# Performance work log

Hardware: AMD Instinct MI355X
Metric: run time of the kernel (lower is better)

The kernel has to match this reference:

```python
import jax, jax.numpy as jnp
import numpy as np

R, D = 8192, 128                  # rays, MPI depth planes (steps per ray)
NX, NY, NZ = 160, 160, 128        # world_size (NZ == mpi_depth)
PDIM, K0, WID, PE = 16, 12, 128, 4
RGBFEA = 4 * (9 + 3 + 3 + 3) + 6  # 78, rgbnet output dim
VSR = 256.0 / D                   # voxel_size_ratio (alpha interval)
LAM = 0.01                        # glob_lambda_den / glob_lambda_rgb


def _act_shift():
    # exact replication of the act_shift buffer init in __init__
    g = np.full([D], 1.0 / D - 1e-6)
    p = [1.0 - g[0]]
    for i in range(1, D):
        p.append((1.0 - g[:i + 1].sum()) / (1.0 - g[:i].sum()))
    p = np.asarray(p)
    return jnp.asarray(np.log(p ** (-1.0 / VSR) - 1.0) - 1.0, dtype=jnp.float32)


def setup_inputs() -> dict:
    key = jax.random.key(0)
    ks = jax.random.split(key, 8)
    dim0 = 3 + 3 * PE * 2 + K0  # 39
    return {
        "rays_o": jax.random.uniform(ks[0], (R, 3), jnp.float32),
        "rays_d": jax.random.normal(ks[1], (R, 3), jnp.float32),
        "density_grid": jax.random.normal(ks[2], (1, NX, NY, NZ), jnp.float32) * 0.1,
        "density_params_grid": jax.random.normal(ks[3], (PDIM, NX, NY, NZ), jnp.float32) * 0.05,
        "k0_grid": jax.random.normal(ks[4], (K0, NX, NY, NZ), jnp.float32) * 0.1,
        "global_flow_den": jnp.zeros((2,), jnp.float32),
        "global_flow_rgb": jnp.zeros((6,), jnp.float32),
        "w0": jax.random.normal(ks[5], (dim0, WID), jnp.float32) / np.sqrt(dim0),
        "b0": jnp.zeros((WID,), jnp.float32),
        "w1": jax.random.normal(ks[6], (WID, WID), jnp.float32) / np.sqrt(WID),
        "b1": jnp.zeros((WID,), jnp.float32),
        "w2": jax.random.normal(ks[7], (WID, RGBFEA), jnp.float32) / np.sqrt(WID),
        "b2": jnp.zeros((RGBFEA,), jnp.float32),
        "act_shift": _act_shift(),  # non-trainable buffer, shape [D]
    }


def _trilinear(grid, pts):
    # grid: [C, X, Y, Z]; pts: [N, 3] in [0, 1] -> returns [N, C]
    sizes_i = np.array(grid.shape[1:], dtype=np.int32)
    sizes_f = jnp.asarray(sizes_i, dtype=pts.dtype)
    g = jnp.clip(pts, 0.0, 1.0) * (sizes_f - 1.0)
    i0 = jnp.clip(jnp.floor(g).astype(jnp.int32), 0, jnp.asarray(sizes_i - 2))
    f = g - i0.astype(pts.dtype)
    out = jnp.zeros((grid.shape[0], pts.shape[0]), dtype=pts.dtype)
    for dx in (0, 1):
        wx = f[:, 0] if dx else 1.0 - f[:, 0]
        for dy in (0, 1):
            wy = f[:, 1] if dy else 1.0 - f[:, 1]
            for dz in (0, 1):
                wz = f[:, 2] if dz else 1.0 - f[:, 2]
                v = grid[:, i0[:, 0] + dx, i0[:, 1] + dy, i0[:, 2] + dz]  # [C, N] gather
                out = out + v * (wx * wy * wz)[None, :]
    return out.T


def reference(rays_o, rays_d, density_grid, density_params_grid, k0_grid,
              global_flow_den, global_flow_rgb, w0, b0, w1, b1, w2, b2, act_shift):
    # --- packed ray sampling over MPI depth planes (create_full_step_id pattern) ---
    t = jnp.linspace(0.0, 1.0, D, dtype=rays_o.dtype)
    pts = rays_o[:, None, :] + rays_d[:, None, :] * t[None, :, None]   # [R, D, 3]
    pts = jnp.clip(pts, 0.0, 1.0).reshape(-1, 3)                        # [R*D, 3]
    ray_id = jnp.repeat(jnp.arange(R, dtype=jnp.int32), D)              # [R*D]
    step_id = jnp.tile(jnp.arange(D, dtype=jnp.int32), R)               # [R*D]

    # --- grid trilinear sampling ---
    density = _trilinear(density_grid, pts)[:, 0]          # [N]
    params = _trilinear(density_params_grid, pts)          # [N, 16]
    k0f = _trilinear(k0_grid, pts)                          # [N, 12]

    # --- per-point normalizing-flow reparam on density (4 flow steps, 4 params each) ---
    z = density + global_flow_den[0] * LAM
    for i in range(4):
        p = params[:, 4 * i:4 * i + 4]
        z = z + p[:, 0] * jnp.tanh(p[:, 1] * z + p[:, 2]) * jax.nn.sigmoid(p[:, 3])

    # --- alpha from shifted density: 1 - exp(-softplus(den + shift) * interval) ---
    den = z + act_shift[step_id]
    alpha = 1.0 - jnp.exp(-jax.nn.softplus(den) * VSR)      # [N]

    # --- per-ray transmittance via exclusive cumprod ---
    a = alpha.reshape(R, D)
    T = jnp.cumprod(1.0 - a + 1e-10, axis=1)
    T_excl = jnp.concatenate([jnp.ones((R, 1), a.dtype), T[:, :-1]], axis=1)
    weights = a * T_excl                                     # [R, D]
    alphainv_last = T[:, -1]                                 # [R]

    # --- view-direction positional encoding, broadcast per point via ray_id gather ---
    viewdirs = rays_d / (jnp.linalg.norm(rays_d, axis=-1, keepdims=True) + 1e-8)
    freq = jnp.asarray([2.0 ** i for i in range(PE)], dtype=rays_d.dtype)
    ang = viewdirs[:, :, None] * freq[None, None, :]          # [R, 3, PE]
    emb = jnp.concatenate([viewdirs, jnp.sin(ang).reshape(R, -1), jnp.cos(ang).reshape(R, -1)], -1)  # [R, 27]

    # --- MLP shading ---
    h = jnp.concatenate([emb[ray_id], k0f], axis=-1)          # [N, 39]
    h = jax.nn.relu(h @ w0 + b0)
    h = jax.nn.relu(h @ w1 + b1)
    feat = h @ w2 + b2                                        # [N, 78]
    rgb = jax.nn.sigmoid(feat[:, :3] + global_flow_rgb[:3] * LAM)  # [N, 3]

    # --- segment-sum compositing over packed ray_id (white background) ---
    wflat = weights.reshape(-1)
    rgb_marched = jax.ops.segment_sum(wflat[:, None] * rgb, ray_id, num_segments=R)
    rgb_marched = rgb_marched + alphainv_last[:, None]
    return rgb_marched
```

## Files before the change

kernel.cpp:

```cpp
#include <hip/hip_runtime.h>
#include <math.h>

#define R_    8192
#define D_    128
#define RD    (R_ * D_)
#define NXg   160
#define NYg   160
#define NZg   128
#define CSg   (NXg * NYg * NZg)
#define WIDm  128
#define K0C   12
#define LAMc  0.01f
#define VSRc  2.0f

#define W1F_N   16384
#define W0KF_N  2048
#define W2F_N   4096
#define WTAB_N  (W1F_N + W0KF_N + W2F_N)
#define LW1     0
#define LW0K    W1F_N
#define LW2     (W1F_N + W0KF_N)

typedef __attribute__((ext_vector_type(8)))  short   short8v;
typedef __attribute__((ext_vector_type(4)))  float   f32x4;
typedef __attribute__((ext_vector_type(16))) float   f32x16;
typedef __attribute__((ext_vector_type(2)))  int     int2v;
typedef __attribute__((ext_vector_type(4)))  int     int4v;
typedef __attribute__((ext_vector_type(4)))  unsigned short ushort4v;
typedef __attribute__((ext_vector_type(8)))  unsigned short ushort8v;

static __device__ __forceinline__ unsigned short f2b(float f) {
    union { float f; unsigned int u; } v; v.f = f;
    unsigned int r = v.u + 0x7fffu + ((v.u >> 16) & 1u);
    return (unsigned short)(r >> 16);
}
static __device__ __forceinline__ float b2f(unsigned short u) {
    union { unsigned int u; float f; } v; v.u = ((unsigned int)u) << 16;
    return v.f;
}
static __device__ __forceinline__ unsigned int pk2(float lo, float hi) {
    unsigned int r;
    asm("v_cvt_pk_bf16_f32 %0, %1, %2" : "=v"(r) : "v"(lo), "v"(hi));
    return r;
}
static __device__ __forceinline__ short8v as_s8(int4v v) {
    union { int4v i; short8v s; } u; u.i = v; return u.s;
}

__global__ __launch_bounds__(256) void k_pack_t(
    const float* __restrict__ dg, const float* __restrict__ pg,
    const float* __restrict__ kg, unsigned short* __restrict__ vox)
{
    const int tid = threadIdx.x;
    const int g   = tid & 3;
    const int s2  = tid >> 2;
    const float* pl[8];
    bool padq[8];
#pragma unroll
    for (int q = 0; q < 8; ++q) {
        int ch = 8 * g + q;
        padq[q] = (ch >= 29);
        pl[q] = (ch == 0) ? dg
              : (ch < 17) ? pg + (size_t)(ch - 1) * CSg
              : (ch < 29) ? kg + (size_t)(ch - 17) * CSg
              : dg;
    }
#pragma unroll
    for (int it = 0; it < 4; ++it) {
        int vofs = (blockIdx.x * 4 + it) * 256 + 4 * s2;
        f32x4 L[8];
#pragma unroll
        for (int q = 0; q < 8; ++q) {
            f32x4 v = __builtin_nontemporal_load((const f32x4*)(pl[q] + vofs));
            if (padq[q]) v = f32x4{0.0f, 0.0f, 0.0f, 0.0f};
            L[q] = v;
        }
#pragma unroll
        for (int k = 0; k < 4; ++k) {
            int4v chunk;
#pragma unroll
            for (int h2 = 0; h2 < 4; ++h2)
                chunk[h2] = (int)pk2(L[2 * h2][k], L[2 * h2 + 1][k]);
            *(int4v*)((char*)vox + (size_t)(vofs + k) * 64 + g * 16) = chunk;
        }
    }
}

__global__ __launch_bounds__(512) void k_prep_all(
    const float* __restrict__ rays_d,
    const float* __restrict__ w0, const float* __restrict__ b0,
    const float* __restrict__ w1, const float* __restrict__ w2,
    float* __restrict__ e, unsigned short* __restrict__ wtab)
{
    int bid = blockIdx.x;
    if (bid < R_ / 4) {
        int r = bid * 4 + (threadIdx.x >> 7);
        int j = threadIdx.x & 127;
        float d0 = rays_d[r * 3 + 0], d1 = rays_d[r * 3 + 1], d2 = rays_d[r * 3 + 2];
        float nrm = sqrtf(d0 * d0 + d1 * d1 + d2 * d2) + 1e-8f;
        float v[3] = { d0 / nrm, d1 / nrm, d2 / nrm };
        float x[27];
        x[0] = v[0]; x[1] = v[1]; x[2] = v[2];
#pragma unroll
        for (int c = 0; c < 3; ++c)
#pragma unroll
            for (int f = 0; f < 4; ++f) {
                float ang = v[c] * (float)(1 << f);
                x[3 + c * 4 + f]  = sinf(ang);
                x[15 + c * 4 + f] = cosf(ang);
            }
        float acc = b0[j];
#pragma unroll
        for (int m = 0; m < 27; ++m) acc = fmaf(x[m], w0[m * WIDm + j], acc);
        e[r * WIDm + j] = acc;
    } else {
        int t = (bid - R_ / 4) * 512 + threadIdx.x;
        if (t < W1F_N) {
            int tile = t >> 9, l = (t >> 3) & 63, j = t & 7;
            int mt = tile >> 3, ks = tile & 7;
            int m = mt * 32 + (l & 31);
            int k = ks * 16 + 8 * (l >> 5) + j;
            wtab[LW1 + t] = f2b(w1[k * WIDm + m]);
        } else if (t < W1F_N + W0KF_N) {
            int u = t - W1F_N;
            int mt = u >> 9, l = (u >> 3) & 63, j = u & 7;
            int m = mt * 32 + (l & 31);
            int k = 8 * (l >> 5) + j;
            wtab[LW0K + u] = f2b(k < K0C ? w0[(27 + k) * WIDm + m] : 0.0f);
        } else if (t < WTAB_N) {
            int u = t - W1F_N - W0KF_N;
            int ks = u >> 9, l = (u >> 3) & 63, j = u & 7;
            int m = l & 31;
            int k = ks * 16 + 8 * (l >> 5) + j;
            wtab[LW2 + u] = f2b(m < 3 ? w2[k * 78 + m] : 0.0f);
        }
    }
}

static __device__ __forceinline__ void sample_coords(
    int sid, const float* __restrict__ rays_o, const float* __restrict__ rays_d,
    int& ix, int& iy, int& iz, float& fx, float& fy, float& fz)
{
    int r = sid >> 7;
    int s = sid & 127;
    float t = s * (1.0f / 127.0f);
    float px = fminf(fmaxf(rays_o[r * 3 + 0] + rays_d[r * 3 + 0] * t, 0.0f), 1.0f);
    float py = fminf(fmaxf(rays_o[r * 3 + 1] + rays_d[r * 3 + 1] * t, 0.0f), 1.0f);
    float pz = fminf(fmaxf(rays_o[r * 3 + 2] + rays_d[r * 3 + 2] * t, 0.0f), 1.0f);
    float gx = px * (float)(NXg - 1);
    float gy = py * (float)(NYg - 1);
    float gz = pz * (float)(NZg - 1);
    ix = min((int)gx, NXg - 2);
    iy = min((int)gy, NYg - 2);
    iz = min((int)gz, NZg - 2);
    fx = gx - (float)ix;
    fy = gy - (float)iy;
    fz = gz - (float)iz;
}

static __device__ __forceinline__ float density_alpha(
    int s, const float* acc, float gfd0, const float* __restrict__ act_shift)
{
    float z = acc[0] + gfd0;
#pragma unroll
    for (int i = 0; i < 4; ++i) {
        float pa = acc[1 + 4 * i + 0], pb = acc[1 + 4 * i + 1];
        float pc = acc[1 + 4 * i + 2], pd = acc[1 + 4 * i + 3];
        float sg = 1.0f / (1.0f + expf(-pd));
        z += pa * tanhf(pb * z + pc) * sg;
    }
    float den = z + act_shift[s];
    float sp = fmaxf(den, 0.0f) + log1pf(expf(-fabsf(den)));
    return 1.0f - expf(-sp * VSRc);
}

static __device__ __forceinline__ void finish_sample(
    int sid, int s, const float* acc, float gfd0,
    const float* __restrict__ act_shift,
    float* __restrict__ alpha_ws, unsigned short* __restrict__ k0b)
{
    alpha_ws[sid] = density_alpha(s, acc, gfd0, act_shift);
    ushort8v lo, hi;
#pragma unroll
    for (int c = 0; c < 8; ++c) lo[c] = f2b(acc[17 + c]);
#pragma unroll
    for (int c = 0; c < 8; ++c) hi[c] = (c < 4) ? f2b(acc[25 + c]) : (unsigned short)0;
    *(ushort8v*)(k0b + (size_t)sid * 16)     = lo;
    *(ushort8v*)(k0b + (size_t)sid * 16 + 8) = hi;
}

__global__ __launch_bounds__(256) void k_gather_aos(
    const float* __restrict__ rays_o, const float* __restrict__ rays_d,
    const unsigned short* __restrict__ vox,
    const float* __restrict__ gfd, const float* __restrict__ act_shift,
    float* __restrict__ alpha_ws, unsigned short* __restrict__ k0b)
{
    int sid = blockIdx.x * 256 + threadIdx.x;
    if (sid >= RD) return;
    int ix, iy, iz; float fx, fy, fz;
    sample_coords(sid, rays_o, rays_d, ix, iy, iz, fx, fy, fz);

    const unsigned short* base = vox + ((size_t)(ix * NYg + iy) * NZg + iz) * 32;
    const size_t qoff[4] = { 0, (size_t)NZg * 32, (size_t)NYg * NZg * 32,
                             (size_t)(NYg + 1) * NZg * 32 };
    float wxy[4];
    wxy[0] = (1.0f - fx) * (1.0f - fy);
    wxy[1] = (1.0f - fx) * fy;
    wxy[2] = fx * (1.0f - fy);
    wxy[3] = fx * fy;
    float wz0 = 1.0f - fz, wz1 = fz;

    float acc[29];
#pragma unroll
    for (int c = 0; c < 29; ++c) acc[c] = 0.0f;

#pragma unroll
    for (int q = 0; q < 4; ++q) {
        const unsigned short* p = base + qoff[q];
#pragma unroll
        for (int dz = 0; dz < 2; ++dz) {
            float w = wxy[q] * (dz ? wz1 : wz0);
            const ushort8v* pv = (const ushort8v*)(p + dz * 32);
            ushort8v v0 = pv[0], v1 = pv[1], v2 = pv[2], v3 = pv[3];
#pragma unroll
            for (int i = 0; i < 8; ++i) acc[i]      = fmaf(w, b2f(v0[i]), acc[i]);
#pragma unroll
            for (int i = 0; i < 8; ++i) acc[8 + i]  = fmaf(w, b2f(v1[i]), acc[8 + i]);
#pragma unroll
            for (int i = 0; i < 8; ++i) acc[16 + i] = fmaf(w, b2f(v2[i]), acc[16 + i]);
#pragma unroll
            for (int i = 0; i < 5; ++i) acc[24 + i] = fmaf(w, b2f(v3[i]), acc[24 + i]);
        }
    }
    finish_sample(sid, sid & 127, acc, gfd[0] * LAMc, act_shift, alpha_ws, k0b);
}

__global__ void k_gather_soa(
    const float* __restrict__ rays_o, const float* __restrict__ rays_d,
    const float* __restrict__ dg,  const float* __restrict__ pg,
    const float* __restrict__ kg,  const float* __restrict__ gfd,
    const float* __restrict__ act_shift,
    float* __restrict__ alpha_ws, unsigned short* __restrict__ k0b)
{
    int sid = blockIdx.x * 256 + threadIdx.x;
    if (sid >= RD) return;
    int ix, iy, iz; float fx, fy, fz;
    sample_coords(sid, rays_o, rays_d, ix, iy, iz, fx, fy, fz);

    int base = (ix * NYg + iy) * NZg + iz;
    int off[4] = { base, base + NZg, base + NYg * NZg, base + NYg * NZg + NZg };
    float wxy[4];
    wxy[0] = (1.0f - fx) * (1.0f - fy);
    wxy[1] = (1.0f - fx) * fy;
    wxy[2] = fx * (1.0f - fy);
    wxy[3] = fx * fy;
    float wz0 = 1.0f - fz, wz1 = fz;

    auto tri = [&](const float* __restrict__ g, int c) -> float {
        float a = 0.0f;
        const float* gc = g + (size_t)c * CSg;
#pragma unroll
        for (int q = 0; q < 4; ++q) {
            const float* p = gc + off[q];
            a += (p[0] * wz0 + p[1] * wz1) * wxy[q];
        }
        return a;
    };
    float acc[29];
    acc[0] = tri(dg, 0);
#pragma unroll
    for (int c = 0; c < 16; ++c) acc[1 + c] = tri(pg, c);
#pragma unroll
    for (int c = 0; c < K0C; ++c) acc[17 + c] = tri(kg, c);
    finish_sample(sid, sid & 127, acc, gfd[0] * LAMc, act_shift, alpha_ws, k0b);
}

struct BPair { int4v lo, hi; };
static __device__ __forceinline__ BPair ttile(const f32x16 v) {
    unsigned p[8];
#pragma unroll
    for (int q = 0; q < 8; ++q) p[q] = pk2(v[2 * q], v[2 * q + 1]);
    int2v a = __builtin_amdgcn_permlane32_swap((int)p[0], (int)p[2], false, false);
    int2v b = __builtin_amdgcn_permlane32_swap((int)p[1], (int)p[3], false, false);
    int2v c = __builtin_amdgcn_permlane32_swap((int)p[4], (int)p[6], false, false);
    int2v d = __builtin_amdgcn_permlane32_swap((int)p[5], (int)p[7], false, false);
    BPair r;
    r.lo = int4v{ a.x, b.x, a.y, b.y };
    r.hi = int4v{ c.x, d.x, c.y, d.y };
    return r;
}

__global__ __launch_bounds__(256) void k_mlp_scan(
    const unsigned short* __restrict__ k0b, const float* __restrict__ e,
    const unsigned short* __restrict__ wtab,
    const float* __restrict__ b1, const float* __restrict__ b2,
    const float* __restrict__ gfr, const float* __restrict__ alpha_ws,
    float* __restrict__ out)
{
    __shared__ unsigned short wlds[WTAB_N];
    __shared__ float rgb_lds[D_][5];
#pragma unroll
    for (int it = 0; it < WTAB_N / (256 * 8); ++it) {
        int i = (it * 256 + threadIdx.x) * 8;
        *(ushort8v*)&wlds[i] = *(const ushort8v*)&wtab[i];
    }
    __syncthreads();

    const int lane = threadIdx.x & 63;
    const int wid  = threadIdx.x >> 6;
    const int n    = lane & 31;
    const int h    = lane >> 5;
    const int ray  = blockIdx.x;
    const int sid  = ray * D_ + wid * 32 + n;

    f32x16 acc0[4];
#pragma unroll
    for (int mt = 0; mt < 4; ++mt) {
        const f32x4* ep = (const f32x4*)(e + (size_t)ray * WIDm + mt * 32 + 4 * h);
#pragma unroll
        for (int rr = 0; rr < 4; ++rr) {
            f32x4 ev = ep[2 * rr];
#pragma unroll
            for (int q = 0; q < 4; ++q) acc0[mt][rr * 4 + q] = ev[q];
        }
    }
    short8v bk = *(const short8v*)(k0b + (size_t)sid * 16 + h * 8);
#pragma unroll
    for (int mt = 0; mt < 4; ++mt) {
        short8v af = *(const short8v*)&wlds[LW0K + (mt * 64 + lane) * 8];
        acc0[mt] = __builtin_amdgcn_mfma_f32_32x32x16_bf16(af, bk, acc0[mt], 0, 0, 0);
    }
    int4v bw[8];
#pragma unroll
    for (int mt = 0; mt < 4; ++mt) {
        f32x16 hv;
#pragma unroll
        for (int r = 0; r < 16; ++r) hv[r] = fmaxf(acc0[mt][r], 0.0f);
        BPair t = ttile(hv);
        bw[2 * mt]     = t.lo;
        bw[2 * mt + 1] = t.hi;
    }

    f32x16 acc1[4];
#pragma unroll
    for (int mt = 0; mt < 4; ++mt) {
        const f32x4* bp = (const f32x4*)(b1 + mt * 32 + 4 * h);
#pragma unroll
        for (int rr = 0; rr < 4; ++rr) {
            f32x4 bv = bp[2 * rr];
#pragma unroll
            for (int q = 0; q < 4; ++q) acc1[mt][rr * 4 + q] = bv[q];
        }
    }
#pragma unroll
    for (int mt = 0; mt < 4; ++mt)
#pragma unroll
        for (int ks = 0; ks < 8; ++ks) {
            short8v af = *(const short8v*)&wlds[LW1 + ((mt * 8 + ks) * 64 + lane) * 8];
            acc1[mt] = __builtin_amdgcn_mfma_f32_32x32x16_bf16(af, as_s8(bw[ks]), acc1[mt], 0, 0, 0);
        }
    int4v cw[8];
#pragma unroll
    for (int mt = 0; mt < 4; ++mt) {
        f32x16 hv;
#pragma unroll
        for (int r = 0; r < 16; ++r) hv[r] = fmaxf(acc1[mt][r], 0.0f);
        BPair t = ttile(hv);
        cw[2 * mt]     = t.lo;
        cw[2 * mt + 1] = t.hi;
    }

    f32x16 acc2;
#pragma unroll
    for (int r = 0; r < 16; ++r) acc2[r] = 0.0f;
#pragma unroll
    for (int ks = 0; ks < 8; ++ks) {
        short8v af = *(const short8v*)&wlds[LW2 + (ks * 64 + lane) * 8];
        acc2 = __builtin_amdgcn_mfma_f32_32x32x16_bf16(af, as_s8(cw[ks]), acc2, 0, 0, 0);
    }
    if (h == 0) {
#pragma unroll
        for (int c = 0; c < 3; ++c) {
            float v = acc2[c] + b2[c] + gfr[c] * LAMc;
            rgb_lds[wid * 32 + n][c] = 1.0f / (1.0f + expf(-v));
        }
    }
    __syncthreads();

    if (wid == 0) {
        int base = ray * D_ + lane * 2;
        float a0 = alpha_ws[base];
        float a1 = alpha_ws[base + 1];
        float q0 = 1.0f - a0 + 1e-10f;
        float q1 = 1.0f - a1 + 1e-10f;
        float p = q0 * q1;

        float incl = p;
#pragma unroll
        for (int o = 1; o < 64; o <<= 1) {
            float v = __shfl_up(incl, o);
            if (lane >= o) incl *= v;
        }
        float excl = __shfl_up(incl, 1);
        if (lane == 0) excl = 1.0f;
        float Tlast = __shfl(incl, 63);

        float w0s = a0 * excl;
        float w1s = a1 * excl * q0;

        float sums[3];
#pragma unroll
        for (int c = 0; c < 3; ++c) {
            float sc = w0s * rgb_lds[2 * lane][c] + w1s * rgb_lds[2 * lane + 1][c];
#pragma unroll
            for (int o = 32; o >= 1; o >>= 1) sc += __shfl_xor(sc, o);
            sums[c] = sc;
        }
        if (lane == 0) {
#pragma unroll
            for (int c = 0; c < 3; ++c) out[ray * 3 + c] = sums[c] + Tlast;
        }
    }
}

extern "C" void kernel_launch(void* const* d_in, const int* in_sizes, int n_in,
                              void* d_out, int out_size, void* d_ws, size_t ws_size,
                              hipStream_t stream) {
    const float* rays_o    = (const float*)d_in[0];
    const float* rays_d    = (const float*)d_in[1];
    const float* dg        = (const float*)d_in[2];
    const float* pg        = (const float*)d_in[3];
    const float* kg        = (const float*)d_in[4];
    const float* gfd       = (const float*)d_in[5];
    const float* gfr       = (const float*)d_in[6];
    const float* w0        = (const float*)d_in[7];
    const float* b0        = (const float*)d_in[8];
    const float* w1        = (const float*)d_in[9];
    const float* b1        = (const float*)d_in[10];
    const float* w2        = (const float*)d_in[11];
    const float* b2        = (const float*)d_in[12];
    const float* act_shift = (const float*)d_in[13];
    float* out = (float*)d_out;

    float* ws = (float*)d_ws;
    float*          alpha_ws = ws;
    unsigned short* k0b      = (unsigned short*)(ws + 4 * (size_t)RD);
    float*          e_ws     = ws + 12 * (size_t)RD;
    unsigned short* wtab     = (unsigned short*)(ws + 13 * (size_t)RD);
    size_t frag_end = 13 * (size_t)RD * 4 + (size_t)WTAB_N * 2;
    size_t vox_off  = (frag_end + 63) & ~(size_t)63;
    unsigned short* vox = (unsigned short*)((char*)d_ws + vox_off);
    size_t need = vox_off + (size_t)CSg * 64;
    bool use_aos = (ws_size >= need);

    k_prep_all<<<dim3(R_ / 4 + (WTAB_N + 511) / 512), dim3(512), 0, stream>>>(
        rays_d, w0, b0, w1, w2, e_ws, wtab);
    if (use_aos) {
        k_pack_t<<<dim3(CSg / 1024), dim3(256), 0, stream>>>(dg, pg, kg, vox);
        k_gather_aos<<<dim3(RD / 256), dim3(256), 0, stream>>>(
            rays_o, rays_d, vox, gfd, act_shift, alpha_ws, k0b);
    } else {
        k_gather_soa<<<dim3(RD / 256), dim3(256), 0, stream>>>(
            rays_o, rays_d, dg, pg, kg, gfd, act_shift, alpha_ws, k0b);
    }
    k_mlp_scan<<<dim3(R_), dim3(256), 0, stream>>>(
        k0b, e_ws, wtab, b1, b2, gfr, alpha_ws, out);
}
```

Before: 255.5 us.

## Merge pack and prep kernels; process one ray per wave in MLP

The voxel pack kernel and the embedding/weight-table prep kernel become a single launch whose block ranges select each role, removing one launch and letting the two run concurrently. The MLP/scan kernel now gives each wave one full ray and loops over four 32-sample tiles. The block-wide syncthreads and the single-wave compositing step go away, and the shared-memory weight table is loaded once per four rays instead of once per ray. In exchange, each block runs longer and serial work per wave grows, with fewer blocks available to hide latency.

```diff
diff --git a/kernel.cpp b/kernel.cpp
--- a/kernel.cpp
+++ b/kernel.cpp
@@ -21,6 +21,10 @@
 #define LW0K    W1F_N
 #define LW2     (W1F_N + W0KF_N)
 
+#define PACK_BLKS   (CSg / 1024)
+#define EPREP_BLKS  (R_ / 2)
+#define WTAB_BLKS   (WTAB_N / 256)
+
 typedef __attribute__((ext_vector_type(8)))  short   short8v;
 typedef __attribute__((ext_vector_type(4)))  float   f32x4;
 typedef __attribute__((ext_vector_type(16))) float   f32x16;
@@ -47,42 +51,103 @@
     union { int4v i; short8v s; } u; u.i = v; return u.s;
 }
 
-__global__ __launch_bounds__(256) void k_pack_t(
+static __device__ __forceinline__ void eprep_body(
+    int r, int j, const float* __restrict__ rays_d,
+    const float* __restrict__ w0, const float* __restrict__ b0, float* __restrict__ e)
+{
+    float d0 = rays_d[r * 3 + 0], d1 = rays_d[r * 3 + 1], d2 = rays_d[r * 3 + 2];
+    float nrm = sqrtf(d0 * d0 + d1 * d1 + d2 * d2) + 1e-8f;
+    float v[3] = { d0 / nrm, d1 / nrm, d2 / nrm };
+    float x[27];
+    x[0] = v[0]; x[1] = v[1]; x[2] = v[2];
+#pragma unroll
+    for (int c = 0; c < 3; ++c)
+#pragma unroll
+        for (int f = 0; f < 4; ++f) {
+            float ang = v[c] * (float)(1 << f);
+            x[3 + c * 4 + f]  = sinf(ang);
+            x[15 + c * 4 + f] = cosf(ang);
+        }
+    float acc = b0[j];
+#pragma unroll
+    for (int m = 0; m < 27; ++m) acc = fmaf(x[m], w0[m * WIDm + j], acc);
+    e[r * WIDm + j] = acc;
+}
+
+static __device__ __forceinline__ void wtab_body(
+    int t, const float* __restrict__ w0, const float* __restrict__ w1,
+    const float* __restrict__ w2, unsigned short* __restrict__ wtab)
+{
+    if (t < W1F_N) {
+        int tile = t >> 9, l = (t >> 3) & 63, j = t & 7;
+        int mt = tile >> 3, ks = tile & 7;
+        int m = mt * 32 + (l & 31);
+        int k = ks * 16 + 8 * (l >> 5) + j;
+        wtab[LW1 + t] = f2b(w1[k * WIDm + m]);
+    } else if (t < W1F_N + W0KF_N) {
+        int u = t - W1F_N;
+        int mt = u >> 9, l = (u >> 3) & 63, j = u & 7;
+        int m = mt * 32 + (l & 31);
+        int k = 8 * (l >> 5) + j;
+        wtab[LW0K + u] = f2b(k < K0C ? w0[(27 + k) * WIDm + m] : 0.0f);
+    } else if (t < WTAB_N) {
+        int u = t - W1F_N - W0KF_N;
+        int ks = u >> 9, l = (u >> 3) & 63, j = u & 7;
+        int m = l & 31;
+        int k = ks * 16 + 8 * (l >> 5) + j;
+        wtab[LW2 + u] = f2b(m < 3 ? w2[k * 78 + m] : 0.0f);
+    }
+}
+
+__global__ __launch_bounds__(256) void k_pack_prep(
     const float* __restrict__ dg, const float* __restrict__ pg,
-    const float* __restrict__ kg, unsigned short* __restrict__ vox)
-{
+    const float* __restrict__ kg, unsigned short* __restrict__ vox,
+    const float* __restrict__ rays_d,
+    const float* __restrict__ w0, const float* __restrict__ b0,
+    const float* __restrict__ w1, const float* __restrict__ w2,
+    float* __restrict__ e, unsigned short* __restrict__ wtab)
+{
+    const int bid = blockIdx.x;
     const int tid = threadIdx.x;
-    const int g   = tid & 3;
-    const int s2  = tid >> 2;
-    const float* pl[8];
-    bool padq[8];
-#pragma unroll
-    for (int q = 0; q < 8; ++q) {
-        int ch = 8 * g + q;
-        padq[q] = (ch >= 29);
-        pl[q] = (ch == 0) ? dg
-              : (ch < 17) ? pg + (size_t)(ch - 1) * CSg
-              : (ch < 29) ? kg + (size_t)(ch - 17) * CSg
-              : dg;
-    }
-#pragma unroll
-    for (int it = 0; it < 4; ++it) {
-        int vofs = (blockIdx.x * 4 + it) * 256 + 4 * s2;
-        f32x4 L[8];
+    if (bid < PACK_BLKS) {
+        const int g   = tid & 3;
+        const int s2  = tid >> 2;
+        const float* pl[8];
+        bool padq[8];
 #pragma unroll
         for (int q = 0; q < 8; ++q) {
-            f32x4 v = __builtin_nontemporal_load((const f32x4*)(pl[q] + vofs));
-            if (padq[q]) v = f32x4{0.0f, 0.0f, 0.0f, 0.0f};
-            L[q] = v;
-        }
-#pragma unroll
-        for (int k = 0; k < 4; ++k) {
-            int4v chunk;
-#pragma unroll
-            for (int h2 = 0; h2 < 4; ++h2)
-                chunk[h2] = (int)pk2(L[2 * h2][k], L[2 * h2 + 1][k]);
-            *(int4v*)((char*)vox + (size_t)(vofs + k) * 64 + g * 16) = chunk;
-        }
+            int ch = 8 * g + q;
+            padq[q] = (ch >= 29);
+            pl[q] = (ch == 0) ? dg
+                  : (ch < 17) ? pg + (size_t)(ch - 1) * CSg
+                  : (ch < 29) ? kg + (size_t)(ch - 17) * CSg
+                  : dg;
+        }
+#pragma unroll
+        for (int it = 0; it < 4; ++it) {
+            int vofs = (bid * 4 + it) * 256 + 4 * s2;
+            f32x4 L[8];
+#pragma unroll
+            for (int q = 0; q < 8; ++q) {
+                f32x4 v = __builtin_nontemporal_load((const f32x4*)(pl[q] + vofs));
+                if (padq[q]) v = f32x4{0.0f, 0.0f, 0.0f, 0.0f};
+                L[q] = v;
+            }
+#pragma unroll
+            for (int k = 0; k < 4; ++k) {
+                int4v chunk;
+#pragma unroll
+                for (int h2 = 0; h2 < 4; ++h2)
+                    chunk[h2] = (int)pk2(L[2 * h2][k], L[2 * h2 + 1][k]);
+                *(int4v*)((char*)vox + (size_t)(vofs + k) * 64 + g * 16) = chunk;
+            }
+        }
+    } else if (bid < PACK_BLKS + EPREP_BLKS) {
+        int r = (bid - PACK_BLKS) * 2 + (tid >> 7);
+        eprep_body(r, tid & 127, rays_d, w0, b0, e);
+    } else {
+        int t = (bid - PACK_BLKS - EPREP_BLKS) * 256 + tid;
+        wtab_body(t, w0, w1, w2, wtab);
     }
 }
 
@@ -95,45 +160,10 @@
     int bid = blockIdx.x;
     if (bid < R_ / 4) {
         int r = bid * 4 + (threadIdx.x >> 7);
-        int j = threadIdx.x & 127;
-        float d0 = rays_d[r * 3 + 0], d1 = rays_d[r * 3 + 1], d2 = rays_d[r * 3 + 2];
-        float nrm = sqrtf(d0 * d0 + d1 * d1 + d2 * d2) + 1e-8f;
-        float v[3] = { d0 / nrm, d1 / nrm, d2 / nrm };
-        float x[27];
-        x[0] = v[0]; x[1] = v[1]; x[2] = v[2];
-#pragma unroll
-        for (int c = 0; c < 3; ++c)
-#pragma unroll
-            for (int f = 0; f < 4; ++f) {
-                float ang = v[c] * (float)(1 << f);
-                x[3 + c * 4 + f]  = sinf(ang);
-                x[15 + c * 4 + f] = cosf(ang);
-            }
-        float acc = b0[j];
-#pragma unroll
-        for (int m = 0; m < 27; ++m) acc = fmaf(x[m], w0[m * WIDm + j], acc);
-        e[r * WIDm + j] = acc;
+        eprep_body(r, threadIdx.x & 127, rays_d, w0, b0, e);
     } else {
         int t = (bid - R_ / 4) * 512 + threadIdx.x;
-        if (t < W1F_N) {
-            int tile = t >> 9, l = (t >> 3) & 63, j = t & 7;
-            int mt = tile >> 3, ks = tile & 7;
-            int m = mt * 32 + (l & 31);
-            int k = ks * 16 + 8 * (l >> 5) + j;
-            wtab[LW1 + t] = f2b(w1[k * WIDm + m]);
-        } else if (t < W1F_N + W0KF_N) {
-            int u = t - W1F_N;
-            int mt = u >> 9, l = (u >> 3) & 63, j = u & 7;
-            int m = mt * 32 + (l & 31);
-            int k = 8 * (l >> 5) + j;
-            wtab[LW0K + u] = f2b(k < K0C ? w0[(27 + k) * WIDm + m] : 0.0f);
-        } else if (t < WTAB_N) {
-            int u = t - W1F_N - W0KF_N;
-            int ks = u >> 9, l = (u >> 3) & 63, j = u & 7;
-            int m = l & 31;
-            int k = ks * 16 + 8 * (l >> 5) + j;
-            wtab[LW2 + u] = f2b(m < 3 ? w2[k * 78 + m] : 0.0f);
-        }
+        wtab_body(t, w0, w1, w2, wtab);
     }
 }
 
@@ -290,7 +320,7 @@
     return r;
 }
 
-__global__ __launch_bounds__(256) void k_mlp_scan(
+__global__ __launch_bounds__(256) void k_mlp_scan4(
     const unsigned short* __restrict__ k0b, const float* __restrict__ e,
     const unsigned short* __restrict__ wtab,
     const float* __restrict__ b1, const float* __restrict__ b2,
@@ -298,7 +328,7 @@
     float* __restrict__ out)
 {
     __shared__ unsigned short wlds[WTAB_N];
-    __shared__ float rgb_lds[D_][5];
+    __shared__ float rgb_lds[4][D_][4];
 #pragma unroll
     for (int it = 0; it < WTAB_N / (256 * 8); ++it) {
         int i = (it * 256 + threadIdx.x) * 8;
@@ -310,116 +340,116 @@
     const int wid  = threadIdx.x >> 6;
     const int n    = lane & 31;
     const int h    = lane >> 5;
-    const int ray  = blockIdx.x;
-    const int sid  = ray * D_ + wid * 32 + n;
-
-    f32x16 acc0[4];
-#pragma unroll
-    for (int mt = 0; mt < 4; ++mt) {
-        const f32x4* ep = (const f32x4*)(e + (size_t)ray * WIDm + mt * 32 + 4 * h);
-#pragma unroll
-        for (int rr = 0; rr < 4; ++rr) {
-            f32x4 ev = ep[2 * rr];
-#pragma unroll
-            for (int q = 0; q < 4; ++q) acc0[mt][rr * 4 + q] = ev[q];
-        }
-    }
-    short8v bk = *(const short8v*)(k0b + (size_t)sid * 16 + h * 8);
-#pragma unroll
-    for (int mt = 0; mt < 4; ++mt) {
-        short8v af = *(const short8v*)&wlds[LW0K + (mt * 64 + lane) * 8];
-        acc0[mt] = __builtin_amdgcn_mfma_f32_32x32x16_bf16(af, bk, acc0[mt], 0, 0, 0);
-    }
-    int4v bw[8];
-#pragma unroll
-    for (int mt = 0; mt < 4; ++mt) {
-        f32x16 hv;
-#pragma unroll
-        for (int r = 0; r < 16; ++r) hv[r] = fmaxf(acc0[mt][r], 0.0f);
-        BPair t = ttile(hv);
-        bw[2 * mt]     = t.lo;
-        bw[2 * mt + 1] = t.hi;
-    }
-
-    f32x16 acc1[4];
-#pragma unroll
-    for (int mt = 0; mt < 4; ++mt) {
-        const f32x4* bp = (const f32x4*)(b1 + mt * 32 + 4 * h);
-#pragma unroll
-        for (int rr = 0; rr < 4; ++rr) {
-            f32x4 bv = bp[2 * rr];
-#pragma unroll
-            for (int q = 0; q < 4; ++q) acc1[mt][rr * 4 + q] = bv[q];
-        }
-    }
-#pragma unroll
-    for (int mt = 0; mt < 4; ++mt)
+    const int ray  = blockIdx.x * 4 + wid;
+
+    for (int t = 0; t < 4; ++t) {
+        const int sid = ray * D_ + t * 32 + n;
+
+        f32x16 acc0[4];
+#pragma unroll
+        for (int mt = 0; mt < 4; ++mt) {
+            const f32x4* ep = (const f32x4*)(e + (size_t)ray * WIDm + mt * 32 + 4 * h);
+#pragma unroll
+            for (int rr = 0; rr < 4; ++rr) {
+                f32x4 ev = ep[2 * rr];
+#pragma unroll
+                for (int q = 0; q < 4; ++q) acc0[mt][rr * 4 + q] = ev[q];
+            }
+        }
+        short8v bk = *(const short8v*)(k0b + (size_t)sid * 16 + h * 8);
+#pragma unroll
+        for (int mt = 0; mt < 4; ++mt) {
+            short8v af = *(const short8v*)&wlds[LW0K + (mt * 64 + lane) * 8];
+            acc0[mt] = __builtin_amdgcn_mfma_f32_32x32x16_bf16(af, bk, acc0[mt], 0, 0, 0);
+        }
+        int4v bw[8];
+#pragma unroll
+        for (int mt = 0; mt < 4; ++mt) {
+            f32x16 hv;
+#pragma unroll
+            for (int r = 0; r < 16; ++r) hv[r] = fmaxf(acc0[mt][r], 0.0f);
+            BPair tt = ttile(hv);
+            bw[2 * mt]     = tt.lo;
+            bw[2 * mt + 1] = tt.hi;
+        }
+
+        f32x16 acc1[4];
+#pragma unroll
+        for (int mt = 0; mt < 4; ++mt) {
+            const f32x4* bp = (const f32x4*)(b1 + mt * 32 + 4 * h);
+#pragma unroll
+            for (int rr = 0; rr < 4; ++rr) {
+                f32x4 bv = bp[2 * rr];
+#pragma unroll
+                for (int q = 0; q < 4; ++q) acc1[mt][rr * 4 + q] = bv[q];
+            }
+        }
+#pragma unroll
+        for (int mt = 0; mt < 4; ++mt)
+#pragma unroll
+            for (int ks = 0; ks < 8; ++ks) {
+                short8v af = *(const short8v*)&wlds[LW1 + ((mt * 8 + ks) * 64 + lane) * 8];
+                acc1[mt] = __builtin_amdgcn_mfma_f32_32x32x16_bf16(af, as_s8(bw[ks]), acc1[mt], 0, 0, 0);
+            }
+        int4v cw[8];
+#pragma unroll
+        for (int mt = 0; mt < 4; ++mt) {
+            f32x16 hv;
+#pragma unroll
+            for (int r = 0; r < 16; ++r) hv[r] = fmaxf(acc1[mt][r], 0.0f);
+            BPair tt = ttile(hv);
+            cw[2 * mt]     = tt.lo;
+            cw[2 * mt + 1] = tt.hi;
+        }
+
+        f32x16 acc2;
+#pragma unroll
+        for (int r = 0; r < 16; ++r) acc2[r] = 0.0f;
 #pragma unroll
         for (int ks = 0; ks < 8; ++ks) {
-            short8v af = *(const short8v*)&wlds[LW1 + ((mt * 8 + ks) * 64 + lane) * 8];
-            acc1[mt] = __builtin_amdgcn_mfma_f32_32x32x16_bf16(af, as_s8(bw[ks]), acc1[mt], 0, 0, 0);
-        }
-    int4v cw[8];
-#pragma unroll
-    for (int mt = 0; mt < 4; ++mt) {
-        f32x16 hv;
-#pragma unroll
-        for (int r = 0; r < 16; ++r) hv[r] = fmaxf(acc1[mt][r], 0.0f);
-        BPair t = ttile(hv);
-        cw[2 * mt]     = t.lo;
-        cw[2 * mt + 1] = t.hi;
-    }
-
-    f32x16 acc2;
-#pragma unroll
-    for (int r = 0; r < 16; ++r) acc2[r] = 0.0f;
-#pragma unroll
-    for (int ks = 0; ks < 8; ++ks) {
-        short8v af = *(const short8v*)&wlds[LW2 + (ks * 64 + lane) * 8];
-        acc2 = __builtin_amdgcn_mfma_f32_32x32x16_bf16(af, as_s8(cw[ks]), acc2, 0, 0, 0);
-    }
-    if (h == 0) {
-#pragma unroll
-        for (int c = 0; c < 3; ++c) {
-            float v = acc2[c] + b2[c] + gfr[c] * LAMc;
-            rgb_lds[wid * 32 + n][c] = 1.0f / (1.0f + expf(-v));
-        }
-    }
-    __syncthreads();
-
-    if (wid == 0) {
-        int base = ray * D_ + lane * 2;
-        float a0 = alpha_ws[base];
-        float a1 = alpha_ws[base + 1];
-        float q0 = 1.0f - a0 + 1e-10f;
-        float q1 = 1.0f - a1 + 1e-10f;
-        float p = q0 * q1;
-
-        float incl = p;
-#pragma unroll
-        for (int o = 1; o < 64; o <<= 1) {
-            float v = __shfl_up(incl, o);
-            if (lane >= o) incl *= v;
-        }
-        float excl = __shfl_up(incl, 1);
-        if (lane == 0) excl = 1.0f;
-        float Tlast = __shfl(incl, 63);
-
-        float w0s = a0 * excl;
-        float w1s = a1 * excl * q0;
-
-        float sums[3];
-#pragma unroll
-        for (int c = 0; c < 3; ++c) {
-            float sc = w0s * rgb_lds[2 * lane][c] + w1s * rgb_lds[2 * lane + 1][c];
-#pragma unroll
-            for (int o = 32; o >= 1; o >>= 1) sc += __shfl_xor(sc, o);
-            sums[c] = sc;
-        }
-        if (lane == 0) {
-#pragma unroll
-            for (int c = 0; c < 3; ++c) out[ray * 3 + c] = sums[c] + Tlast;
-        }
+            short8v af = *(const short8v*)&wlds[LW2 + (ks * 64 + lane) * 8];
+            acc2 = __builtin_amdgcn_mfma_f32_32x32x16_bf16(af, as_s8(cw[ks]), acc2, 0, 0, 0);
+        }
+        if (h == 0) {
+#pragma unroll
+            for (int c = 0; c < 3; ++c) {
+                float v = acc2[c] + b2[c] + gfr[c] * LAMc;
+                rgb_lds[wid][t * 32 + n][c] = 1.0f / (1.0f + expf(-v));
+            }
+        }
+    }
+
+    int base = ray * D_ + lane * 2;
+    float a0 = alpha_ws[base];
+    float a1 = alpha_ws[base + 1];
+    float q0 = 1.0f - a0 + 1e-10f;
+    float q1 = 1.0f - a1 + 1e-10f;
+    float p = q0 * q1;
+
+    float incl = p;
+#pragma unroll
+    for (int o = 1; o < 64; o <<= 1) {
+        float v = __shfl_up(incl, o);
+        if (lane >= o) incl *= v;
+    }
+    float excl = __shfl_up(incl, 1);
+    if (lane == 0) excl = 1.0f;
+    float Tlast = __shfl(incl, 63);
+
+    float w0s = a0 * excl;
+    float w1s = a1 * excl * q0;
+
+    float sums[3];
+#pragma unroll
+    for (int c = 0; c < 3; ++c) {
+        float sc = w0s * rgb_lds[wid][2 * lane][c] + w1s * rgb_lds[wid][2 * lane + 1][c];
+#pragma unroll
+        for (int o = 32; o >= 1; o >>= 1) sc += __shfl_xor(sc, o);
+        sums[c] = sc;
+    }
+    if (lane == 0) {
+#pragma unroll
+        for (int c = 0; c < 3; ++c) out[ray * 3 + c] = sums[c] + Tlast;
     }
 }
 
@@ -453,16 +483,17 @@
     size_t need = vox_off + (size_t)CSg * 64;
     bool use_aos = (ws_size >= need);
 
-    k_prep_all<<<dim3(R_ / 4 + (WTAB_N + 511) / 512), dim3(512), 0, stream>>>(
-        rays_d, w0, b0, w1, w2, e_ws, wtab);
     if (use_aos) {
-        k_pack_t<<<dim3(CSg / 1024), dim3(256), 0, stream>>>(dg, pg, kg, vox);
+        k_pack_prep<<<dim3(PACK_BLKS + EPREP_BLKS + WTAB_BLKS), dim3(256), 0, stream>>>(
+            dg, pg, kg, vox, rays_d, w0, b0, w1, w2, e_ws, wtab);
         k_gather_aos<<<dim3(RD / 256), dim3(256), 0, stream>>>(
             rays_o, rays_d, vox, gfd, act_shift, alpha_ws, k0b);
     } else {
+        k_prep_all<<<dim3(R_ / 4 + (WTAB_N + 511) / 512), dim3(512), 0, stream>>>(
+            rays_d, w0, b0, w1, w2, e_ws, wtab);
         k_gather_soa<<<dim3(RD / 256), dim3(256), 0, stream>>>(
             rays_o, rays_d, dg, pg, kg, gfd, act_shift, alpha_ws, k0b);
     }
-    k_mlp_scan<<<dim3(R_), dim3(256), 0, stream>>>(
+    k_mlp_scan4<<<dim3(R_ / 4), dim3(256), 0, stream>>>(
         k0b, e_ws, wtab, b1, b2, gfr, alpha_ws, out);
 }
```

Result: faster. 240.9 us (-5.7%).
